# Kernel tuning notes

Hardware: AMD Instinct MI355X
Metric: run time of the kernel (lower is better)

## Reference

```python
import jax, jax.numpy as jnp
import numpy as np

EPS = 1e-12  # matches torch F.normalize default eps
SCALE = 64.0  # fixed softmax temperature from the source

def _l2_normalize(x, axis):
    n = jnp.linalg.norm(x, ord=2, axis=axis, keepdims=True)
    return x / jnp.maximum(n, EPS)

def setup_inputs() -> dict:
    key = jax.random.key(0)
    k1, k2, k3 = jax.random.split(key, 3)
    B, L, S, D = 8, 2048, 2048, 128
    return {
        "query": jax.random.normal(k1, (B, L, D), dtype=jnp.float32),
        "key": jax.random.normal(k2, (B, S, D), dtype=jnp.float32),
        "value": jax.random.normal(k3, (B, S, D), dtype=jnp.float32),
    }

def reference(query, key, value):
    # rank-3 query path with norm=True, return_value=True, return_score=False
    q = _l2_normalize(query, axis=2)   # [B, L, D]
    k = _l2_normalize(key, axis=2)     # [B, S, D]
    score = jnp.einsum('nlk,nsk->nls', q, k)            # [B, L, S]
    score = jax.nn.softmax(score * SCALE, axis=2)
    # original does broadcast-multiply-then-sum; equivalent contraction:
    out = jnp.einsum('nls,nsd->nld', score, value)      # [B, L, D]
    return out
```

## Files before the change

kernel.cpp:

```cpp
#include <hip/hip_runtime.h>
#include <stdint.h>

#define Bb 8
#define Ll 2048
#define Ss 2048
#define Dd 128
#define NSB 4
#define SCHUNK 512
#define NROWS 16384
#define SCALE_LOG2E 92.33248261689366f

typedef __attribute__((ext_vector_type(8))) short bf16x8;
typedef __attribute__((ext_vector_type(16))) float f32x16;

__device__ __forceinline__ unsigned f2bf_pack(float a, float b) {
  unsigned ua = __float_as_uint(a); ua += 0x7fffu + ((ua >> 16) & 1u);
  unsigned ub = __float_as_uint(b); ub += 0x7fffu + ((ub >> 16) & 1u);
  return (ua >> 16) | (ub & 0xffff0000u);
}

__device__ __forceinline__ unsigned pkbf(float a, float b) {
#if __has_builtin(__builtin_amdgcn_cvt_pk_bf16_f32)
  auto r = __builtin_amdgcn_cvt_pk_bf16_f32(a, b);
  return __builtin_bit_cast(unsigned, r);
#else
  return f2bf_pack(a, b);
#endif
}

__device__ __forceinline__ void gl_lds16(const void* g, void* l) {
  __builtin_amdgcn_global_load_lds(
      (const __attribute__((address_space(1))) unsigned*)g,
      (__attribute__((address_space(3))) unsigned*)l, 16, 0, 0);
}


extern "C" __global__ __launch_bounds__(256)
void prep_kern(const float* __restrict__ Q, const float* __restrict__ K,
               const float* __restrict__ V,
               unsigned short* __restrict__ Qn, unsigned short* __restrict__ Kf,
               unsigned short* __restrict__ Vf) {
  __shared__ float Tf[32 * 130];
  __shared__ float Ps[32 * 8];
  __shared__ float Nr[32];
  __shared__ unsigned short Tb[32 * 128];
  const int t = threadIdx.x;
  const int bid = blockIdx.x;
  if (bid < 4096) {
    const int lane = t & 63;
    const int r = bid * 4 + (t >> 6);
    float2 f = *(const float2*)(Q + (size_t)r * Dd + lane * 2);
    float ss = f.x * f.x + f.y * f.y;
#pragma unroll
    for (int m = 1; m < 64; m <<= 1) ss += __shfl_xor(ss, m, 64);
    float inv = 1.0f / fmaxf(sqrtf(ss), 1e-12f);
    *(unsigned*)(Qn + (size_t)r * Dd + lane * 2) = pkbf(f.x * inv, f.y * inv);
  } else if (bid < 4608) {
    const int kb = bid - 4096;
    const int b = kb & 7, sw = kb >> 3;
    const int sl = t >> 3, d0 = (t & 7) * 16;
    const float* src = K + ((size_t)(b * Ss + sw * 32 + sl)) * Dd + d0;
    float ss = 0.f;
#pragma unroll
    for (int i = 0; i < 4; ++i) {
      float4 v = *(const float4*)(src + i * 4);
      Tf[sl * 130 + d0 + i * 4 + 0] = v.x;
      Tf[sl * 130 + d0 + i * 4 + 1] = v.y;
      Tf[sl * 130 + d0 + i * 4 + 2] = v.z;
      Tf[sl * 130 + d0 + i * 4 + 3] = v.w;
      ss += v.x * v.x + v.y * v.y + v.z * v.z + v.w * v.w;
    }
    Ps[sl * 8 + (t & 7)] = ss;
    __syncthreads();
    if (t < 32) {
      float s = 0.f;
#pragma unroll
      for (int j = 0; j < 8; ++j) s += Ps[t * 8 + j];
      Nr[t] = 1.0f / fmaxf(sqrtf(s), 1e-12f);
    }
    __syncthreads();
    unsigned short* Ko = Kf + ((size_t)(b * 64 + sw)) * 4096;
#pragma unroll
    for (int p = 0; p < 2; ++p) {
      const int run = p * 256 + t;
      const int lane = run & 63, s = lane & 31, h = lane >> 5;
      const int d = (run >> 6) * 16 + h * 8;
      const float n = Nr[s];
      const float* row = &Tf[s * 130 + d];
      uint4 w;
      w.x = pkbf(row[0] * n, row[1] * n);
      w.y = pkbf(row[2] * n, row[3] * n);
      w.z = pkbf(row[4] * n, row[5] * n);
      w.w = pkbf(row[6] * n, row[7] * n);
      *(uint4*)(Ko + run * 8) = w;
    }
  } else {
    const int vb = bid - 4608;
    const int b = vb & 7, sw = vb >> 3;
    const int sl = t >> 3, d0 = (t & 7) * 16;
    const float* src = V + ((size_t)(b * Ss + sw * 32 + sl)) * Dd + d0;
#pragma unroll
    for (int i = 0; i < 4; ++i) {
      float4 v = *(const float4*)(src + i * 4);
      *(unsigned*)&Tb[sl * 128 + d0 + i * 4]     = pkbf(v.x, v.y);
      *(unsigned*)&Tb[sl * 128 + d0 + i * 4 + 2] = pkbf(v.z, v.w);
    }
    __syncthreads();
    unsigned short* Vo = Vf + ((size_t)(b * 64 + sw)) * 4096;
#pragma unroll
    for (int p = 0; p < 2; ++p) {
      const int run = p * 256 + t;
      const int vslot = run >> 6, lane = run & 63;
      const int dloc = lane & 31, h = lane >> 5;
      const int dblk = vslot >> 1, t2 = vslot & 1;
      const int d = dblk * 32 + dloc;
      unsigned short w[8];
#pragma unroll
      for (int j = 0; j < 8; ++j) {
        const int sloc = t2 * 16 + 4 * h + (j & 3) + 8 * (j >> 2);
        w[j] = Tb[sloc * 128 + d];
      }
      *(uint4*)(Vo + run * 8) = *(uint4*)w;
    }
  }
}

extern "C" __global__ __launch_bounds__(256, 2)
void attn_kern(const unsigned short* __restrict__ Qn,
               const unsigned short* __restrict__ Kf,
               const unsigned short* __restrict__ Vf,
               unsigned short* __restrict__ Op,
               float* __restrict__ Lp) {
  __shared__ unsigned short Kl[2][16 * 512];
  __shared__ unsigned short Vl[2][16 * 512];
  const int tid = threadIdx.x, wv = tid >> 6, lane = tid & 63;
  const int lm = lane & 31, h = lane >> 5;
  const int gid = blockIdx.x;
  const int qt = gid >> 5, b = (gid >> 2) & 7, sb = gid & 3;
  const int sblk0 = sb * (SCHUNK / 32);
  const int qrow = qt * 128 + wv * 32 + lm;

  const unsigned short* Qrow = Qn + ((size_t)(b * Ll + qrow)) * Dd;
  bf16x8 qf[8];
#pragma unroll
  for (int kt = 0; kt < 8; ++kt)
    qf[kt] = *(const bf16x8*)(Qrow + kt * 16 + h * 8);

  const unsigned short* Kc = Kf + ((size_t)(b * 64 + sblk0)) * 4096;
  const unsigned short* Vc = Vf + ((size_t)(b * 64 + sblk0)) * 4096;

  f32x16 o[4];
#pragma unroll
  for (int i = 0; i < 4; ++i)
#pragma unroll
    for (int r = 0; r < 16; ++r) o[i][r] = 0.f;

  auto stage = [&](int it, int buf) {
#pragma unroll
    for (int i = 0; i < 4; ++i) {
      const int sl = wv * 4 + i;
      gl_lds16(Kc + (size_t)(it * 2 + (sl >> 3)) * 4096 + (sl & 7) * 512 + lane * 8,
               &Kl[buf][sl * 512]);
      gl_lds16(Vc + (size_t)(it * 2 + (sl >> 3)) * 4096 + (sl & 7) * 512 + lane * 8,
               &Vl[buf][sl * 512]);
    }
  };
  stage(0, 0);

  float lrun = 0.f;

#pragma unroll 1
  for (int it = 0; it < 8; ++it) {
    __syncthreads();
    const int cur = it & 1;
    if (it + 1 < 8) stage(it + 1, cur ^ 1);

#pragma unroll
    for (int sblk = 0; sblk < 2; ++sblk) {
      f32x16 acc;
#pragma unroll
      for (int r = 0; r < 16; ++r) acc[r] = 0.f;
#pragma unroll
      for (int kt = 0; kt < 8; ++kt) {
        bf16x8 kf = *(const bf16x8*)&Kl[cur][(sblk * 8 + kt) * 512 + lane * 8];
        acc = __builtin_amdgcn_mfma_f32_32x32x16_bf16(kf, qf[kt], acc, 0, 0, 0);
      }
#pragma unroll
      for (int t2 = 0; t2 < 2; ++t2) {
        float p[8];
#pragma unroll
        for (int j = 0; j < 8; ++j)
          p[j] = __builtin_amdgcn_exp2f(
              __builtin_fmaf(acc[t2 * 8 + j], SCALE_LOG2E, -SCALE_LOG2E));
        lrun += ((p[0] + p[1]) + (p[2] + p[3])) + ((p[4] + p[5]) + (p[6] + p[7]));
        uint4 fr;
        fr.x = pkbf(p[0], p[1]);
        fr.y = pkbf(p[2], p[3]);
        fr.z = pkbf(p[4], p[5]);
        fr.w = pkbf(p[6], p[7]);
        bf16x8 pf = __builtin_bit_cast(bf16x8, fr);
#pragma unroll
        for (int dblk = 0; dblk < 4; ++dblk) {
          bf16x8 vf =
              *(const bf16x8*)&Vl[cur][(sblk * 8 + dblk * 2 + t2) * 512 + lane * 8];
          o[dblk] = __builtin_amdgcn_mfma_f32_32x32x16_bf16(vf, pf, o[dblk], 0, 0, 0);
        }
      }
    }
  }

  const float lt = lrun + __shfl_xor(lrun, 32, 64);
  unsigned short* Ob = Op + ((size_t)sb * NROWS + b * Ll + qrow) * Dd;
#pragma unroll
  for (int dblk = 0; dblk < 4; ++dblk)
#pragma unroll
    for (int g = 0; g < 4; ++g) {
      uint2 w;
      w.x = pkbf(o[dblk][g * 4 + 0], o[dblk][g * 4 + 1]);
      w.y = pkbf(o[dblk][g * 4 + 2], o[dblk][g * 4 + 3]);
      *(uint2*)(Ob + dblk * 32 + g * 8 + h * 4) = w;
    }
  if (h == 0) Lp[sb * NROWS + b * Ll + qrow] = lt;
}

extern "C" __global__ __launch_bounds__(256)
void comb_kern(const unsigned short* __restrict__ Op,
               const float* __restrict__ Lp, float* __restrict__ Out) {
  const int idx = blockIdx.x * 256 + threadIdx.x;
  const int row = idx >> 5;
  const int dof = (idx & 31) * 4;
  float den = 0.f;
#pragma unroll
  for (int s = 0; s < NSB; ++s) den += Lp[s * NROWS + row];
  float a0 = 0.f, a1 = 0.f, a2 = 0.f, a3 = 0.f;
#pragma unroll
  for (int s = 0; s < NSB; ++s) {
    uint2 v = *(const uint2*)(Op + ((size_t)s * NROWS + row) * Dd + dof);
    a0 += __uint_as_float(v.x << 16);
    a1 += __uint_as_float(v.x & 0xffff0000u);
    a2 += __uint_as_float(v.y << 16);
    a3 += __uint_as_float(v.y & 0xffff0000u);
  }
  const float inv = 1.f / den;
  float4 r; r.x = a0 * inv; r.y = a1 * inv; r.z = a2 * inv; r.w = a3 * inv;
  *(float4*)(Out + (size_t)row * Dd + dof) = r;
}

extern "C" void kernel_launch(void* const* d_in, const int* in_sizes, int n_in,
                              void* d_out, int out_size, void* d_ws, size_t ws_size,
                              hipStream_t stream) {
  const float* Q = (const float*)d_in[0];
  const float* K = (const float*)d_in[1];
  const float* V = (const float*)d_in[2];
  float* Out = (float*)d_out;
  unsigned short* Qn = (unsigned short*)d_ws;
  unsigned short* Kf = Qn + (size_t)NROWS * Dd;
  unsigned short* Vf = Kf + (size_t)NROWS * Dd;
  unsigned short* Op = Vf + (size_t)Bb * Dd * Ss;
  float* Lp = (float*)(Op + (size_t)NSB * NROWS * Dd);
  hipLaunchKernelGGL(prep_kern, dim3(4096 + 512 + 512), dim3(256), 0, stream,
                     Q, K, V, Qn, Kf, Vf);
  hipLaunchKernelGGL(attn_kern, dim3(512), dim3(256), 0, stream, Qn, Kf, Vf, Op, Lp);
  hipLaunchKernelGGL(comb_kern, dim3(2048), dim3(256), 0, stream, Op, Lp, Out);
}
```

Measured before the change: 107.2 us.

## Process two query tiles per wave and split keys into eight chunks

Each wave now computes two 32-row query tiles, so every K and V fragment read from LDS feeds two MFMAs. Blocks shrink to two waves covering 128 query rows, and the key axis is split into eight 256-wide chunks, giving 1024 blocks. Staging is split so one wave loads K and the other loads V. In exchange, register pressure roughly doubles for accumulators and Q fragments, and the combine kernel reads twice as many partial outputs.

```diff
diff --git a/kernel.cpp b/kernel.cpp
--- a/kernel.cpp
+++ b/kernel.cpp
@@ -5,8 +5,8 @@
 #define Ll 2048
 #define Ss 2048
 #define Dd 128
-#define NSB 4
-#define SCHUNK 512
+#define NSB 8
+#define SCHUNK 256
 #define NROWS 16384
 #define SCALE_LOG2E 92.33248261689366f
 
@@ -125,49 +125,51 @@
   }
 }
 
-extern "C" __global__ __launch_bounds__(256, 2)
+extern "C" __global__ __launch_bounds__(128, 2)
 void attn_kern(const unsigned short* __restrict__ Qn,
                const unsigned short* __restrict__ Kf,
                const unsigned short* __restrict__ Vf,
                unsigned short* __restrict__ Op,
                float* __restrict__ Lp) {
-  __shared__ unsigned short Kl[2][16 * 512];
-  __shared__ unsigned short Vl[2][16 * 512];
+  __shared__ unsigned short Kl[2][8 * 512];
+  __shared__ unsigned short Vl[2][8 * 512];
   const int tid = threadIdx.x, wv = tid >> 6, lane = tid & 63;
   const int lm = lane & 31, h = lane >> 5;
   const int gid = blockIdx.x;
-  const int qt = gid >> 5, b = (gid >> 2) & 7, sb = gid & 3;
+  const int qt = gid >> 6, b = (gid >> 3) & 7, sb = gid & 7;
   const int sblk0 = sb * (SCHUNK / 32);
-  const int qrow = qt * 128 + wv * 32 + lm;
-
-  const unsigned short* Qrow = Qn + ((size_t)(b * Ll + qrow)) * Dd;
-  bf16x8 qf[8];
-#pragma unroll
-  for (int kt = 0; kt < 8; ++kt)
-    qf[kt] = *(const bf16x8*)(Qrow + kt * 16 + h * 8);
-
+  const int qrow = qt * 128 + wv * 64 + lm;
+
+  bf16x8 qf0[8], qf1[8];
+  {
+    const unsigned short* Qr0 = Qn + ((size_t)(b * Ll + qrow)) * Dd;
+#pragma unroll
+    for (int kt = 0; kt < 8; ++kt) {
+      qf0[kt] = *(const bf16x8*)(Qr0 + kt * 16 + h * 8);
+      qf1[kt] = *(const bf16x8*)(Qr0 + 32 * Dd + kt * 16 + h * 8);
+    }
+  }
   const unsigned short* Kc = Kf + ((size_t)(b * 64 + sblk0)) * 4096;
   const unsigned short* Vc = Vf + ((size_t)(b * 64 + sblk0)) * 4096;
 
-  f32x16 o[4];
+  f32x16 o0[4], o1[4];
 #pragma unroll
   for (int i = 0; i < 4; ++i)
 #pragma unroll
-    for (int r = 0; r < 16; ++r) o[i][r] = 0.f;
+    for (int r = 0; r < 16; ++r) { o0[i][r] = 0.f; o1[i][r] = 0.f; }
 
   auto stage = [&](int it, int buf) {
 #pragma unroll
-    for (int i = 0; i < 4; ++i) {
-      const int sl = wv * 4 + i;
-      gl_lds16(Kc + (size_t)(it * 2 + (sl >> 3)) * 4096 + (sl & 7) * 512 + lane * 8,
-               &Kl[buf][sl * 512]);
-      gl_lds16(Vc + (size_t)(it * 2 + (sl >> 3)) * 4096 + (sl & 7) * 512 + lane * 8,
-               &Vl[buf][sl * 512]);
+    for (int i = 0; i < 8; ++i) {
+      if (wv == 0)
+        gl_lds16(Kc + (size_t)it * 4096 + i * 512 + lane * 8, &Kl[buf][i * 512]);
+      else
+        gl_lds16(Vc + (size_t)it * 4096 + i * 512 + lane * 8, &Vl[buf][i * 512]);
     }
   };
   stage(0, 0);
 
-  float lrun = 0.f;
+  float l0 = 0.f, l1 = 0.f;
 
 #pragma unroll 1
   for (int it = 0; it < 8; ++it) {
@@ -175,52 +177,63 @@
     const int cur = it & 1;
     if (it + 1 < 8) stage(it + 1, cur ^ 1);
 
-#pragma unroll
-    for (int sblk = 0; sblk < 2; ++sblk) {
-      f32x16 acc;
-#pragma unroll
-      for (int r = 0; r < 16; ++r) acc[r] = 0.f;
-#pragma unroll
-      for (int kt = 0; kt < 8; ++kt) {
-        bf16x8 kf = *(const bf16x8*)&Kl[cur][(sblk * 8 + kt) * 512 + lane * 8];
-        acc = __builtin_amdgcn_mfma_f32_32x32x16_bf16(kf, qf[kt], acc, 0, 0, 0);
+    f32x16 a0, a1;
+#pragma unroll
+    for (int r = 0; r < 16; ++r) { a0[r] = 0.f; a1[r] = 0.f; }
+#pragma unroll
+    for (int kt = 0; kt < 8; ++kt) {
+      bf16x8 kf = *(const bf16x8*)&Kl[cur][kt * 512 + lane * 8];
+      a0 = __builtin_amdgcn_mfma_f32_32x32x16_bf16(kf, qf0[kt], a0, 0, 0, 0);
+      a1 = __builtin_amdgcn_mfma_f32_32x32x16_bf16(kf, qf1[kt], a1, 0, 0, 0);
+    }
+
+#pragma unroll
+    for (int t2 = 0; t2 < 2; ++t2) {
+      float p0[8], p1[8];
+#pragma unroll
+      for (int j = 0; j < 8; ++j) {
+        p0[j] = __builtin_amdgcn_exp2f(
+            __builtin_fmaf(a0[t2 * 8 + j], SCALE_LOG2E, -SCALE_LOG2E));
+        p1[j] = __builtin_amdgcn_exp2f(
+            __builtin_fmaf(a1[t2 * 8 + j], SCALE_LOG2E, -SCALE_LOG2E));
       }
-#pragma unroll
-      for (int t2 = 0; t2 < 2; ++t2) {
-        float p[8];
-#pragma unroll
-        for (int j = 0; j < 8; ++j)
-          p[j] = __builtin_amdgcn_exp2f(
-              __builtin_fmaf(acc[t2 * 8 + j], SCALE_LOG2E, -SCALE_LOG2E));
-        lrun += ((p[0] + p[1]) + (p[2] + p[3])) + ((p[4] + p[5]) + (p[6] + p[7]));
-        uint4 fr;
-        fr.x = pkbf(p[0], p[1]);
-        fr.y = pkbf(p[2], p[3]);
-        fr.z = pkbf(p[4], p[5]);
-        fr.w = pkbf(p[6], p[7]);
-        bf16x8 pf = __builtin_bit_cast(bf16x8, fr);
-#pragma unroll
-        for (int dblk = 0; dblk < 4; ++dblk) {
-          bf16x8 vf =
-              *(const bf16x8*)&Vl[cur][(sblk * 8 + dblk * 2 + t2) * 512 + lane * 8];
-          o[dblk] = __builtin_amdgcn_mfma_f32_32x32x16_bf16(vf, pf, o[dblk], 0, 0, 0);
-        }
+      l0 += ((p0[0] + p0[1]) + (p0[2] + p0[3])) + ((p0[4] + p0[5]) + (p0[6] + p0[7]));
+      l1 += ((p1[0] + p1[1]) + (p1[2] + p1[3])) + ((p1[4] + p1[5]) + (p1[6] + p1[7]));
+      uint4 f0, f1;
+      f0.x = pkbf(p0[0], p0[1]); f0.y = pkbf(p0[2], p0[3]);
+      f0.z = pkbf(p0[4], p0[5]); f0.w = pkbf(p0[6], p0[7]);
+      f1.x = pkbf(p1[0], p1[1]); f1.y = pkbf(p1[2], p1[3]);
+      f1.z = pkbf(p1[4], p1[5]); f1.w = pkbf(p1[6], p1[7]);
+      bf16x8 pf0 = __builtin_bit_cast(bf16x8, f0);
+      bf16x8 pf1 = __builtin_bit_cast(bf16x8, f1);
+#pragma unroll
+      for (int dblk = 0; dblk < 4; ++dblk) {
+        bf16x8 vf = *(const bf16x8*)&Vl[cur][(dblk * 2 + t2) * 512 + lane * 8];
+        o0[dblk] = __builtin_amdgcn_mfma_f32_32x32x16_bf16(vf, pf0, o0[dblk], 0, 0, 0);
+        o1[dblk] = __builtin_amdgcn_mfma_f32_32x32x16_bf16(vf, pf1, o1[dblk], 0, 0, 0);
       }
     }
   }
 
-  const float lt = lrun + __shfl_xor(lrun, 32, 64);
-  unsigned short* Ob = Op + ((size_t)sb * NROWS + b * Ll + qrow) * Dd;
+  const float lt0 = l0 + __shfl_xor(l0, 32, 64);
+  const float lt1 = l1 + __shfl_xor(l1, 32, 64);
+  unsigned short* Ob0 = Op + ((size_t)sb * NROWS + b * Ll + qrow) * Dd;
 #pragma unroll
   for (int dblk = 0; dblk < 4; ++dblk)
 #pragma unroll
     for (int g = 0; g < 4; ++g) {
-      uint2 w;
-      w.x = pkbf(o[dblk][g * 4 + 0], o[dblk][g * 4 + 1]);
-      w.y = pkbf(o[dblk][g * 4 + 2], o[dblk][g * 4 + 3]);
-      *(uint2*)(Ob + dblk * 32 + g * 8 + h * 4) = w;
-    }
-  if (h == 0) Lp[sb * NROWS + b * Ll + qrow] = lt;
+      uint2 w0, w1;
+      w0.x = pkbf(o0[dblk][g * 4 + 0], o0[dblk][g * 4 + 1]);
+      w0.y = pkbf(o0[dblk][g * 4 + 2], o0[dblk][g * 4 + 3]);
+      w1.x = pkbf(o1[dblk][g * 4 + 0], o1[dblk][g * 4 + 1]);
+      w1.y = pkbf(o1[dblk][g * 4 + 2], o1[dblk][g * 4 + 3]);
+      *(uint2*)(Ob0 + dblk * 32 + g * 8 + h * 4) = w0;
+      *(uint2*)(Ob0 + (size_t)32 * Dd + dblk * 32 + g * 8 + h * 4) = w1;
+    }
+  if (h == 0) {
+    Lp[sb * NROWS + b * Ll + qrow] = lt0;
+    Lp[sb * NROWS + b * Ll + qrow + 32] = lt1;
+  }
 }
 
 extern "C" __global__ __launch_bounds__(256)
@@ -260,6 +273,6 @@
   float* Lp = (float*)(Op + (size_t)NSB * NROWS * Dd);
   hipLaunchKernelGGL(prep_kern, dim3(4096 + 512 + 512), dim3(256), 0, stream,
                      Q, K, V, Qn, Kf, Vf);
-  hipLaunchKernelGGL(attn_kern, dim3(512), dim3(256), 0, stream, Qn, Kf, Vf, Op, Lp);
+  hipLaunchKernelGGL(attn_kern, dim3(1024), dim3(128), 0, stream, Qn, Kf, Vf, Op, Lp);
   hipLaunchKernelGGL(comb_kern, dim3(2048), dim3(256), 0, stream, Op, Lp, Out);
 }
```

Result: slower. 113.6 us (+6.0%).

## Deepen K/V LDS pipeline to four smaller buffers with prefetch distance two

Applied to the files above, without the earlier changes.

Replaces the double-buffered 64-key K/V stages with a four-slot ring of 32-key stages. Loads run two iterations ahead, and explicit s_waitcnt vmcnt plus s_barrier let later prefetches stay in flight instead of draining all outstanding loads. The aim is to hide global-to-LDS latency better while keeping total LDS the same. The cost is twice as many barrier iterations, and correctness now depends on hand-written vmcnt accounting.

```diff
diff --git a/kernel.cpp b/kernel.cpp
--- a/kernel.cpp
+++ b/kernel.cpp
@@ -131,8 +131,8 @@
                const unsigned short* __restrict__ Vf,
                unsigned short* __restrict__ Op,
                float* __restrict__ Lp) {
-  __shared__ unsigned short Kl[2][16 * 512];
-  __shared__ unsigned short Vl[2][16 * 512];
+  __shared__ unsigned short Kl[4][8 * 512];
+  __shared__ unsigned short Vl[4][8 * 512];
   const int tid = threadIdx.x, wv = tid >> 6, lane = tid & 63;
   const int lm = lane & 31, h = lane >> 5;
   const int gid = blockIdx.x;
@@ -155,56 +155,56 @@
 #pragma unroll
     for (int r = 0; r < 16; ++r) o[i][r] = 0.f;
 
-  auto stage = [&](int it, int buf) {
-#pragma unroll
-    for (int i = 0; i < 4; ++i) {
-      const int sl = wv * 4 + i;
-      gl_lds16(Kc + (size_t)(it * 2 + (sl >> 3)) * 4096 + (sl & 7) * 512 + lane * 8,
-               &Kl[buf][sl * 512]);
-      gl_lds16(Vc + (size_t)(it * 2 + (sl >> 3)) * 4096 + (sl & 7) * 512 + lane * 8,
-               &Vl[buf][sl * 512]);
+  auto stage = [&](int t, int r) {
+    const unsigned short* kb = Kc + (size_t)t * 4096;
+    const unsigned short* vb = Vc + (size_t)t * 4096;
+#pragma unroll
+    for (int i = 0; i < 2; ++i) {
+      const int sl = wv * 2 + i;
+      gl_lds16(kb + sl * 512 + lane * 8, &Kl[r][sl * 512]);
+      gl_lds16(vb + sl * 512 + lane * 8, &Vl[r][sl * 512]);
     }
   };
   stage(0, 0);
+  stage(1, 1);
 
   float lrun = 0.f;
 
 #pragma unroll 1
-  for (int it = 0; it < 8; ++it) {
-    __syncthreads();
-    const int cur = it & 1;
-    if (it + 1 < 8) stage(it + 1, cur ^ 1);
-
-#pragma unroll
-    for (int sblk = 0; sblk < 2; ++sblk) {
-      f32x16 acc;
-#pragma unroll
-      for (int r = 0; r < 16; ++r) acc[r] = 0.f;
-#pragma unroll
-      for (int kt = 0; kt < 8; ++kt) {
-        bf16x8 kf = *(const bf16x8*)&Kl[cur][(sblk * 8 + kt) * 512 + lane * 8];
-        acc = __builtin_amdgcn_mfma_f32_32x32x16_bf16(kf, qf[kt], acc, 0, 0, 0);
-      }
-#pragma unroll
-      for (int t2 = 0; t2 < 2; ++t2) {
-        float p[8];
-#pragma unroll
-        for (int j = 0; j < 8; ++j)
-          p[j] = __builtin_amdgcn_exp2f(
-              __builtin_fmaf(acc[t2 * 8 + j], SCALE_LOG2E, -SCALE_LOG2E));
-        lrun += ((p[0] + p[1]) + (p[2] + p[3])) + ((p[4] + p[5]) + (p[6] + p[7]));
-        uint4 fr;
-        fr.x = pkbf(p[0], p[1]);
-        fr.y = pkbf(p[2], p[3]);
-        fr.z = pkbf(p[4], p[5]);
-        fr.w = pkbf(p[6], p[7]);
-        bf16x8 pf = __builtin_bit_cast(bf16x8, fr);
-#pragma unroll
-        for (int dblk = 0; dblk < 4; ++dblk) {
-          bf16x8 vf =
-              *(const bf16x8*)&Vl[cur][(sblk * 8 + dblk * 2 + t2) * 512 + lane * 8];
-          o[dblk] = __builtin_amdgcn_mfma_f32_32x32x16_bf16(vf, pf, o[dblk], 0, 0, 0);
-        }
+  for (int it = 0; it < 16; ++it) {
+    if (it < 15)
+      asm volatile("s_waitcnt vmcnt(4)\n\ts_barrier" ::: "memory");
+    else
+      asm volatile("s_waitcnt vmcnt(0)\n\ts_barrier" ::: "memory");
+    const int r = it & 3;
+    if (it + 2 < 16) stage(it + 2, (it + 2) & 3);
+
+    f32x16 acc;
+#pragma unroll
+    for (int rr = 0; rr < 16; ++rr) acc[rr] = 0.f;
+#pragma unroll
+    for (int kt = 0; kt < 8; ++kt) {
+      bf16x8 kf = *(const bf16x8*)&Kl[r][kt * 512 + lane * 8];
+      acc = __builtin_amdgcn_mfma_f32_32x32x16_bf16(kf, qf[kt], acc, 0, 0, 0);
+    }
+#pragma unroll
+    for (int t2 = 0; t2 < 2; ++t2) {
+      float p[8];
+#pragma unroll
+      for (int j = 0; j < 8; ++j)
+        p[j] = __builtin_amdgcn_exp2f(
+            __builtin_fmaf(acc[t2 * 8 + j], SCALE_LOG2E, -SCALE_LOG2E));
+      lrun += ((p[0] + p[1]) + (p[2] + p[3])) + ((p[4] + p[5]) + (p[6] + p[7]));
+      uint4 fr;
+      fr.x = pkbf(p[0], p[1]);
+      fr.y = pkbf(p[2], p[3]);
+      fr.z = pkbf(p[4], p[5]);
+      fr.w = pkbf(p[6], p[7]);
+      bf16x8 pf = __builtin_bit_cast(bf16x8, fr);
+#pragma unroll
+      for (int dblk = 0; dblk < 4; ++dblk) {
+        bf16x8 vf = *(const bf16x8*)&Vl[r][(dblk * 2 + t2) * 512 + lane * 8];
+        o[dblk] = __builtin_amdgcn_mfma_f32_32x32x16_bf16(vf, pf, o[dblk], 0, 0, 0);
       }
     }
   }
```

Measured after the change: 106.4 us. No clear change (-0.7%).

## Warp-specialize attention: producer waves compute softmax P, consumer waves accumulate PV

Applied to the files above, without the earlier changes.

Splits each block's four waves into two roles. Two waves compute QK^T scores and exponentials and write P tiles to shared memory. The other two waves read P one step later and run the PV MFMAs, so the score and output phases of consecutive key tiles are software-pipelined. Each block now covers 64 query rows, the grid doubles, and launch bounds allow four blocks per CU to raise occupancy. The cost is an extra LDS round trip for P, a barrier every tile, and half as many query rows per block, which means more K/V reloads per query row.

```diff
diff --git a/kernel.cpp b/kernel.cpp
--- a/kernel.cpp
+++ b/kernel.cpp
@@ -125,102 +125,129 @@
   }
 }
 
-extern "C" __global__ __launch_bounds__(256, 2)
+extern "C" __global__ __launch_bounds__(256, 4)
 void attn_kern(const unsigned short* __restrict__ Qn,
                const unsigned short* __restrict__ Kf,
                const unsigned short* __restrict__ Vf,
                unsigned short* __restrict__ Op,
                float* __restrict__ Lp) {
-  __shared__ unsigned short Kl[2][16 * 512];
-  __shared__ unsigned short Vl[2][16 * 512];
+  __shared__ unsigned short Kl[2][8 * 512];
+  __shared__ unsigned short Vl[2][8 * 512];
+  __shared__ unsigned short Pl[2][2][1024];
   const int tid = threadIdx.x, wv = tid >> 6, lane = tid & 63;
   const int lm = lane & 31, h = lane >> 5;
   const int gid = blockIdx.x;
   const int qt = gid >> 5, b = (gid >> 2) & 7, sb = gid & 3;
-  const int sblk0 = sb * (SCHUNK / 32);
-  const int qrow = qt * 128 + wv * 32 + lm;
-
-  const unsigned short* Qrow = Qn + ((size_t)(b * Ll + qrow)) * Dd;
-  bf16x8 qf[8];
-#pragma unroll
-  for (int kt = 0; kt < 8; ++kt)
-    qf[kt] = *(const bf16x8*)(Qrow + kt * 16 + h * 8);
+  const int sblk0 = sb * 16;
+  const bool isA = wv < 2;
+  const int g = wv & 1;
+  const int qrow = qt * 64 + g * 32 + lm;
 
   const unsigned short* Kc = Kf + ((size_t)(b * 64 + sblk0)) * 4096;
   const unsigned short* Vc = Vf + ((size_t)(b * 64 + sblk0)) * 4096;
 
+  bf16x8 qf[8];
   f32x16 o[4];
-#pragma unroll
-  for (int i = 0; i < 4; ++i)
-#pragma unroll
-    for (int r = 0; r < 16; ++r) o[i][r] = 0.f;
-
-  auto stage = [&](int it, int buf) {
-#pragma unroll
-    for (int i = 0; i < 4; ++i) {
-      const int sl = wv * 4 + i;
-      gl_lds16(Kc + (size_t)(it * 2 + (sl >> 3)) * 4096 + (sl & 7) * 512 + lane * 8,
-               &Kl[buf][sl * 512]);
-      gl_lds16(Vc + (size_t)(it * 2 + (sl >> 3)) * 4096 + (sl & 7) * 512 + lane * 8,
-               &Vl[buf][sl * 512]);
-    }
-  };
-  stage(0, 0);
-
+  if (isA) {
+    const unsigned short* Qrow = Qn + ((size_t)(b * Ll + qrow)) * Dd;
+#pragma unroll
+    for (int kt = 0; kt < 8; ++kt)
+      qf[kt] = *(const bf16x8*)(Qrow + kt * 16 + h * 8);
+  } else {
+#pragma unroll
+    for (int i = 0; i < 4; ++i)
+#pragma unroll
+      for (int r = 0; r < 16; ++r) o[i][r] = 0.f;
+  }
   float lrun = 0.f;
 
+  auto stageK = [&](int t) {
+    const unsigned short* kb = Kc + (size_t)t * 4096;
+#pragma unroll
+    for (int i = 0; i < 4; ++i) {
+      const int sl = g * 4 + i;
+      gl_lds16(kb + sl * 512 + lane * 8, &Kl[t & 1][sl * 512]);
+    }
+  };
+  auto stageV = [&](int t) {
+    const unsigned short* vb = Vc + (size_t)t * 4096;
+#pragma unroll
+    for (int i = 0; i < 4; ++i) {
+      const int sl = g * 4 + i;
+      gl_lds16(vb + sl * 512 + lane * 8, &Vl[t & 1][sl * 512]);
+    }
+  };
+
+  auto computeS = [&](int t) {
+    const int buf = t & 1;
+    f32x16 acc;
+#pragma unroll
+    for (int r = 0; r < 16; ++r) acc[r] = 0.f;
+#pragma unroll
+    for (int kt = 0; kt < 8; ++kt) {
+      bf16x8 kf = *(const bf16x8*)&Kl[buf][kt * 512 + lane * 8];
+      acc = __builtin_amdgcn_mfma_f32_32x32x16_bf16(kf, qf[kt], acc, 0, 0, 0);
+    }
+#pragma unroll
+    for (int t2 = 0; t2 < 2; ++t2) {
+      float p[8];
+#pragma unroll
+      for (int j = 0; j < 8; ++j)
+        p[j] = __builtin_amdgcn_exp2f(
+            __builtin_fmaf(acc[t2 * 8 + j], SCALE_LOG2E, -SCALE_LOG2E));
+      lrun += ((p[0] + p[1]) + (p[2] + p[3])) + ((p[4] + p[5]) + (p[6] + p[7]));
+      uint4 fr;
+      fr.x = pkbf(p[0], p[1]);
+      fr.y = pkbf(p[2], p[3]);
+      fr.z = pkbf(p[4], p[5]);
+      fr.w = pkbf(p[6], p[7]);
+      *(uint4*)&Pl[buf][g][(t2 * 64 + lane) * 8] = fr;
+    }
+  };
+  auto computeO = [&](int t) {
+    const int buf = t & 1;
+#pragma unroll
+    for (int t2 = 0; t2 < 2; ++t2) {
+      bf16x8 pf = *(const bf16x8*)&Pl[buf][g][(t2 * 64 + lane) * 8];
+#pragma unroll
+      for (int dblk = 0; dblk < 4; ++dblk) {
+        bf16x8 vf = *(const bf16x8*)&Vl[buf][(dblk * 2 + t2) * 512 + lane * 8];
+        o[dblk] = __builtin_amdgcn_mfma_f32_32x32x16_bf16(vf, pf, o[dblk], 0, 0, 0);
+      }
+    }
+  };
+
+  if (isA) { stageK(0); stageK(1); } else { stageV(0); }
+  asm volatile("s_waitcnt vmcnt(0)\n\ts_barrier" ::: "memory");
+  if (isA) computeS(0);
+
 #pragma unroll 1
-  for (int it = 0; it < 8; ++it) {
-    __syncthreads();
-    const int cur = it & 1;
-    if (it + 1 < 8) stage(it + 1, cur ^ 1);
-
-#pragma unroll
-    for (int sblk = 0; sblk < 2; ++sblk) {
-      f32x16 acc;
-#pragma unroll
-      for (int r = 0; r < 16; ++r) acc[r] = 0.f;
-#pragma unroll
-      for (int kt = 0; kt < 8; ++kt) {
-        bf16x8 kf = *(const bf16x8*)&Kl[cur][(sblk * 8 + kt) * 512 + lane * 8];
-        acc = __builtin_amdgcn_mfma_f32_32x32x16_bf16(kf, qf[kt], acc, 0, 0, 0);
+  for (int t = 0; t < 16; ++t) {
+    asm volatile("s_waitcnt vmcnt(0) lgkmcnt(0)\n\ts_barrier" ::: "memory");
+    if (isA) {
+      if (t + 2 < 16) stageK(t + 2);
+      if (t + 1 < 16) computeS(t + 1);
+    } else {
+      if (t + 1 < 16) stageV(t + 1);
+      computeO(t);
+    }
+  }
+
+  if (isA) {
+    const float lt = lrun + __shfl_xor(lrun, 32, 64);
+    if (h == 0) Lp[sb * NROWS + b * Ll + qrow] = lt;
+  } else {
+    unsigned short* Ob = Op + ((size_t)sb * NROWS + b * Ll + qrow) * Dd;
+#pragma unroll
+    for (int dblk = 0; dblk < 4; ++dblk)
+#pragma unroll
+      for (int gg = 0; gg < 4; ++gg) {
+        uint2 w;
+        w.x = pkbf(o[dblk][gg * 4 + 0], o[dblk][gg * 4 + 1]);
+        w.y = pkbf(o[dblk][gg * 4 + 2], o[dblk][gg * 4 + 3]);
+        *(uint2*)(Ob + dblk * 32 + gg * 8 + h * 4) = w;
       }
-#pragma unroll
-      for (int t2 = 0; t2 < 2; ++t2) {
-        float p[8];
-#pragma unroll
-        for (int j = 0; j < 8; ++j)
-          p[j] = __builtin_amdgcn_exp2f(
-              __builtin_fmaf(acc[t2 * 8 + j], SCALE_LOG2E, -SCALE_LOG2E));
-        lrun += ((p[0] + p[1]) + (p[2] + p[3])) + ((p[4] + p[5]) + (p[6] + p[7]));
-        uint4 fr;
-        fr.x = pkbf(p[0], p[1]);
-        fr.y = pkbf(p[2], p[3]);
-        fr.z = pkbf(p[4], p[5]);
-        fr.w = pkbf(p[6], p[7]);
-        bf16x8 pf = __builtin_bit_cast(bf16x8, fr);
-#pragma unroll
-        for (int dblk = 0; dblk < 4; ++dblk) {
-          bf16x8 vf =
-              *(const bf16x8*)&Vl[cur][(sblk * 8 + dblk * 2 + t2) * 512 + lane * 8];
-          o[dblk] = __builtin_amdgcn_mfma_f32_32x32x16_bf16(vf, pf, o[dblk], 0, 0, 0);
-        }
-      }
-    }
-  }
-
-  const float lt = lrun + __shfl_xor(lrun, 32, 64);
-  unsigned short* Ob = Op + ((size_t)sb * NROWS + b * Ll + qrow) * Dd;
-#pragma unroll
-  for (int dblk = 0; dblk < 4; ++dblk)
-#pragma unroll
-    for (int g = 0; g < 4; ++g) {
-      uint2 w;
-      w.x = pkbf(o[dblk][g * 4 + 0], o[dblk][g * 4 + 1]);
-      w.y = pkbf(o[dblk][g * 4 + 2], o[dblk][g * 4 + 3]);
-      *(uint2*)(Ob + dblk * 32 + g * 8 + h * 4) = w;
-    }
-  if (h == 0) Lp[sb * NROWS + b * Ll + qrow] = lt;
+  }
 }
 
 extern "C" __global__ __launch_bounds__(256)
@@ -260,6 +287,6 @@
   float* Lp = (float*)(Op + (size_t)NSB * NROWS * Dd);
   hipLaunchKernelGGL(prep_kern, dim3(4096 + 512 + 512), dim3(256), 0, stream,
                      Q, K, V, Qn, Kf, Vf);
-  hipLaunchKernelGGL(attn_kern, dim3(512), dim3(256), 0, stream, Qn, Kf, Vf, Op, Lp);
+  hipLaunchKernelGGL(attn_kern, dim3(1024), dim3(256), 0, stream, Qn, Kf, Vf, Op, Lp);
   hipLaunchKernelGGL(comb_kern, dim3(2048), dim3(256), 0, stream, Op, Lp, Out);
 }
```

New measurement: 115.2 us. 1.07x slower.
